# Kernel optimization log

Hardware: AMD Instinct MI355X
Metric: run time of the kernel (lower is better)

Reference implementation:

```python
import jax, jax.numpy as jnp
import numpy as np

K = 11          # k_size in the original module
HALF = K // 2   # 5
N_SIGNAL = 33554432  # 2**25 elements, 128 MB fp32


def setup_inputs() -> dict:
    key = jax.random.key(0)
    k1, _ = jax.random.split(key)
    x = jax.random.normal(k1, (N_SIGNAL,), dtype=jnp.float32)
    # learned parameter of Dilation1D(s=1.5)
    scale = jnp.asarray(1.5, dtype=jnp.float32)
    return {"x": x, "scale": scale}


def reference(x, scale):
    # parabolic structuring element: z = -5..5, h = -z^2 / (4*scale)
    z = jnp.linspace(-(K // 2), K // 2, K, dtype=jnp.float32)  # torch: -k//2+1 .. k//2 == -5..5
    h = -(z * z) / (4.0 * scale)  # [K]

    n = x.shape[0]
    pad = jnp.full((HALF,), -jnp.inf, dtype=x.dtype)
    xp = jnp.concatenate([pad, x, pad])  # [n + K - 1], -inf edge handling == original branches

    # out[r] = max_j ( x[r - HALF + j] + h[j] )  (max-plus / grayscale dilation)
    out = xp[0:n] + h[0]
    for j in range(1, K):  # fixed small K, unrolled window — no data-dim loop
        out = jnp.maximum(out, xp[j:j + n] + h[j])
    return out
```

## Files before the change

### kernel.cpp

```cpp
#include <hip/hip_runtime.h>
#include <math.h>


#define KSZ 11
#define HALF 5
#define VEC 16
#define NLOAD 8

__global__ __launch_bounds__(256) void dilate1d_kernel(
    const float4* __restrict__ x4,
    const float*  __restrict__ scale_p,
    float4*       __restrict__ out4,
    int n4)
{
    const float s = scale_p[0];
    float h[KSZ];
#pragma unroll
    for (int j = 0; j < KSZ; ++j) {
        float z = (float)(j - HALF);
        h[j] = -(z * z) / (4.0f * s);
    }

    int q0 = (blockIdx.x * blockDim.x + threadIdx.x) * (VEC / 4);
    if (q0 >= n4) return;

    const float NEG = -INFINITY;

    float xs[NLOAD * 4];
#pragma unroll
    for (int t = 0; t < NLOAD; ++t) {
        int q = q0 - 2 + t;
        float4 v;
        if (q >= 0 && q < n4) {
            v = x4[q];
        } else {
            v = make_float4(NEG, NEG, NEG, NEG);
        }
        xs[4 * t + 0] = v.x;
        xs[4 * t + 1] = v.y;
        xs[4 * t + 2] = v.z;
        xs[4 * t + 3] = v.w;
    }

#pragma unroll
    for (int t = 0; t < VEC / 4; ++t) {
        if (q0 + t >= n4) break;
        float4 o;
        float* op = &o.x;
#pragma unroll
        for (int i = 0; i < 4; ++i) {
            int c = 8 + 4 * t + i;
            float m = xs[c - HALF] + h[0];
#pragma unroll
            for (int j = 1; j < KSZ; ++j) {
                m = fmaxf(m, xs[c - HALF + j] + h[j]);
            }
            op[i] = m;
        }
        out4[q0 + t] = o;
    }
}

extern "C" void kernel_launch(void* const* d_in, const int* in_sizes, int n_in,
                              void* d_out, int out_size, void* d_ws, size_t ws_size,
                              hipStream_t stream) {
    const float* x       = (const float*)d_in[0];
    const float* scale_p = (const float*)d_in[1];
    float*       out     = (float*)d_out;

    int n  = in_sizes[0];
    int n4 = n / 4;

    int threads_needed = (n4 + (VEC / 4) - 1) / (VEC / 4);
    int block = 256;
    int grid  = (threads_needed + block - 1) / block;

    dilate1d_kernel<<<grid, block, 0, stream>>>(
        (const float4*)x, scale_p, (float4*)out, n4);
}
```

Before: 243.6 us.

## Use grid-stride loop with one coalesced float4 output per thread iteration

Each thread now produces one float4 per iteration of a grid-stride loop, instead of four contiguous float4 outputs. Adjacent lanes then read and write adjacent float4s, which coalesces memory accesses better than the earlier per-thread 64-byte stride. An unchecked fast path covers interior elements so bounds checks run only at the edges. The cost is that each thread loads a 5-float4 halo per output float4, so redundant reads go through the caches rather than being reused in registers.

```diff
diff --git a/kernel.cpp b/kernel.cpp
--- a/kernel.cpp
+++ b/kernel.cpp
@@ -2,10 +2,9 @@
 #include <math.h>
 
 
-#define KSZ 11
+#define KSZ  11
 #define HALF 5
-#define VEC 16
-#define NLOAD 8
+#define ITER 4
 
 __global__ __launch_bounds__(256) void dilate1d_kernel(
     const float4* __restrict__ x4,
@@ -21,35 +20,40 @@
         h[j] = -(z * z) / (4.0f * s);
     }
 
-    int q0 = (blockIdx.x * blockDim.x + threadIdx.x) * (VEC / 4);
-    if (q0 >= n4) return;
+    const float NEG = -INFINITY;
+    const int stride = gridDim.x * blockDim.x;
 
-    const float NEG = -INFINITY;
+    for (int q = blockIdx.x * blockDim.x + threadIdx.x; q < n4; q += stride) {
+        float xs[20];
 
-    float xs[NLOAD * 4];
+        if (q >= 2 && q + 2 < n4) {
 #pragma unroll
-    for (int t = 0; t < NLOAD; ++t) {
-        int q = q0 - 2 + t;
-        float4 v;
-        if (q >= 0 && q < n4) {
-            v = x4[q];
+            for (int t = 0; t < 5; ++t) {
+                float4 v = x4[q - 2 + t];
+                xs[4 * t + 0] = v.x;
+                xs[4 * t + 1] = v.y;
+                xs[4 * t + 2] = v.z;
+                xs[4 * t + 3] = v.w;
+            }
         } else {
-            v = make_float4(NEG, NEG, NEG, NEG);
+#pragma unroll
+            for (int t = 0; t < 5; ++t) {
+                int qq = q - 2 + t;
+                float4 v;
+                if (qq >= 0 && qq < n4) v = x4[qq];
+                else                    v = make_float4(NEG, NEG, NEG, NEG);
+                xs[4 * t + 0] = v.x;
+                xs[4 * t + 1] = v.y;
+                xs[4 * t + 2] = v.z;
+                xs[4 * t + 3] = v.w;
+            }
         }
-        xs[4 * t + 0] = v.x;
-        xs[4 * t + 1] = v.y;
-        xs[4 * t + 2] = v.z;
-        xs[4 * t + 3] = v.w;
-    }
 
-#pragma unroll
-    for (int t = 0; t < VEC / 4; ++t) {
-        if (q0 + t >= n4) break;
         float4 o;
         float* op = &o.x;
 #pragma unroll
         for (int i = 0; i < 4; ++i) {
-            int c = 8 + 4 * t + i;
+            int c = 8 + i;
             float m = xs[c - HALF] + h[0];
 #pragma unroll
             for (int j = 1; j < KSZ; ++j) {
@@ -57,7 +61,7 @@
             }
             op[i] = m;
         }
-        out4[q0 + t] = o;
+        out4[q] = o;
     }
 }
 
@@ -71,9 +75,9 @@
     int n  = in_sizes[0];
     int n4 = n / 4;
 
-    int threads_needed = (n4 + (VEC / 4) - 1) / (VEC / 4);
     int block = 256;
-    int grid  = (threads_needed + block - 1) / block;
+    long long threads_wanted = (long long)(n4 + ITER - 1) / ITER;
+    int grid = (int)((threads_wanted + block - 1) / block);
 
     dilate1d_kernel<<<grid, block, 0, stream>>>(
         (const float4*)x, scale_p, (float4*)out, n4);
```

New measurement: 231.1 us. -5.1%, faster.

## Use coalesced per-thread float4 pairs with halo scalars and symmetric max-plus

Applied to the files above, without the earlier changes.

Each thread now computes two float4 outputs spaced half the array apart instead of four consecutive float4s. Every load across a warp becomes a unit-stride float4 (plus the neighbour vectors and two scalar halo elements), which removes the strided per-thread access of the old mapping. The inner loop exploits the symmetry of the parabolic element, taking the max of the paired neighbours before adding the shared offset, which roughly halves the adds. The cost is more redundant halo loads per output, which the caches must absorb, and less per-thread reuse of loaded data.

```diff
diff --git a/kernel.cpp b/kernel.cpp
--- a/kernel.cpp
+++ b/kernel.cpp
@@ -2,63 +2,88 @@
 #include <math.h>
 
 
-#define KSZ 11
 #define HALF 5
-#define VEC 16
-#define NLOAD 8
 
 __global__ __launch_bounds__(256) void dilate1d_kernel(
-    const float4* __restrict__ x4,
+    const float*  __restrict__ x,
     const float*  __restrict__ scale_p,
     float4*       __restrict__ out4,
-    int n4)
+    int n4,
+    int T)
 {
     const float s = scale_p[0];
-    float h[KSZ];
-#pragma unroll
-    for (int j = 0; j < KSZ; ++j) {
-        float z = (float)(j - HALF);
-        h[j] = -(z * z) / (4.0f * s);
-    }
-
-    int q0 = (blockIdx.x * blockDim.x + threadIdx.x) * (VEC / 4);
-    if (q0 >= n4) return;
+    float hp1 = -1.0f  / (4.0f * s);
+    float hp2 = -4.0f  / (4.0f * s);
+    float hp3 = -9.0f  / (4.0f * s);
+    float hp4 = -16.0f / (4.0f * s);
+    float hp5 = -25.0f / (4.0f * s);
 
     const float NEG = -INFINITY;
+    const float4 NEG4 = make_float4(NEG, NEG, NEG, NEG);
+    const float4* x4 = (const float4*)x;
 
-    float xs[NLOAD * 4];
-#pragma unroll
-    for (int t = 0; t < NLOAD; ++t) {
-        int q = q0 - 2 + t;
-        float4 v;
-        if (q >= 0 && q < n4) {
-            v = x4[q];
-        } else {
-            v = make_float4(NEG, NEG, NEG, NEG);
-        }
-        xs[4 * t + 0] = v.x;
-        xs[4 * t + 1] = v.y;
-        xs[4 * t + 2] = v.z;
-        xs[4 * t + 3] = v.w;
-    }
+    const int qA = blockIdx.x * blockDim.x + threadIdx.x;
+    const int qB = qA + T;
+    const bool hasB = (qB < n4);
 
-#pragma unroll
-    for (int t = 0; t < VEC / 4; ++t) {
-        if (q0 + t >= n4) break;
-        float4 o;
-        float* op = &o.x;
+    float4 amid = x4[qA];
+    float4 alo  = (qA >= 1)      ? x4[qA - 1] : NEG4;
+    float4 ahi  = (qA + 1 < n4)  ? x4[qA + 1] : NEG4;
+    float  axl  = (qA >= 2)      ? x[4 * qA - 5] : NEG;
+    float  axr  = (qA + 2 < n4)  ? x[4 * qA + 8] : NEG;
+    float4 bmid = hasB               ? x4[qB]     : NEG4;
+    float4 blo  = (qB >= 1 && hasB)  ? x4[qB - 1] : NEG4;
+    float4 bhi  = (qB + 1 < n4)      ? x4[qB + 1] : NEG4;
+    float  bxl  = (qB >= 2 && hasB)  ? x[4 * qB - 5] : NEG;
+    float  bxr  = (qB + 2 < n4)      ? x[4 * qB + 8] : NEG;
+
+    float w[14];
+    float hparr[6];
+    hparr[1] = hp1; hparr[2] = hp2; hparr[3] = hp3; hparr[4] = hp4; hparr[5] = hp5;
+
+    w[0] = axl;
+    w[1] = alo.x;  w[2] = alo.y;  w[3] = alo.z;  w[4] = alo.w;
+    w[5] = amid.x; w[6] = amid.y; w[7] = amid.z; w[8] = amid.w;
+    w[9] = ahi.x;  w[10] = ahi.y; w[11] = ahi.z; w[12] = ahi.w;
+    w[13] = axr;
+
+    float4 oA;
+    {
+        float* op = &oA.x;
 #pragma unroll
         for (int i = 0; i < 4; ++i) {
-            int c = 8 + 4 * t + i;
-            float m = xs[c - HALF] + h[0];
+            int c = HALF + i;
+            float m = w[c];
 #pragma unroll
-            for (int j = 1; j < KSZ; ++j) {
-                m = fmaxf(m, xs[c - HALF + j] + h[j]);
+            for (int d = 1; d <= HALF; ++d) {
+                m = fmaxf(m, hparr[d] + fmaxf(w[c - d], w[c + d]));
             }
             op[i] = m;
         }
-        out4[q0 + t] = o;
     }
+    out4[qA] = oA;
+
+    w[0] = bxl;
+    w[1] = blo.x;  w[2] = blo.y;  w[3] = blo.z;  w[4] = blo.w;
+    w[5] = bmid.x; w[6] = bmid.y; w[7] = bmid.z; w[8] = bmid.w;
+    w[9] = bhi.x;  w[10] = bhi.y; w[11] = bhi.z; w[12] = bhi.w;
+    w[13] = bxr;
+
+    float4 oB;
+    {
+        float* op = &oB.x;
+#pragma unroll
+        for (int i = 0; i < 4; ++i) {
+            int c = HALF + i;
+            float m = w[c];
+#pragma unroll
+            for (int d = 1; d <= HALF; ++d) {
+                m = fmaxf(m, hparr[d] + fmaxf(w[c - d], w[c + d]));
+            }
+            op[i] = m;
+        }
+    }
+    if (hasB) out4[qB] = oB;
 }
 
 extern "C" void kernel_launch(void* const* d_in, const int* in_sizes, int n_in,
@@ -70,11 +95,11 @@
 
     int n  = in_sizes[0];
     int n4 = n / 4;
+    int T  = (n4 + 1) / 2;
 
-    int threads_needed = (n4 + (VEC / 4) - 1) / (VEC / 4);
     int block = 256;
-    int grid  = (threads_needed + block - 1) / block;
+    int grid  = (T + block - 1) / block;
 
     dilate1d_kernel<<<grid, block, 0, stream>>>(
-        (const float4*)x, scale_p, (float4*)out, n4);
+        x, scale_p, (float4*)out, n4, T);
 }
```

After: 275.4 us. 1.13x slower.
